# Performance work log

Measured on AMD Instinct MI355X. Metric: run time of the kernel, lower is better.

The kernel has to match this reference:

```python
import jax, jax.numpy as jnp
import numpy as np

N_NODES = 50000
N_EDGES = 800000
D = 96
DEPTH = 2


def setup_inputs() -> dict:
    key = jax.random.key(0)
    ks = jax.random.split(key, 8)
    scale = 1.0 / np.sqrt(D)
    x = jax.random.normal(ks[0], (N_NODES, D), dtype=jnp.float32)
    W0 = jax.random.normal(ks[1], (DEPTH, D, D), dtype=jnp.float32) * scale
    b0 = jnp.zeros((DEPTH, D), dtype=jnp.float32)
    W1 = jax.random.normal(ks[2], (DEPTH, D, D), dtype=jnp.float32) * scale
    b1 = jnp.zeros((DEPTH, D), dtype=jnp.float32)
    W2 = jax.random.normal(ks[3], (DEPTH, 2 * D, D), dtype=jnp.float32) * (1.0 / np.sqrt(2 * D))
    b2 = jnp.zeros((DEPTH, D), dtype=jnp.float32)
    edge_src = jax.random.randint(ks[4], (N_EDGES,), 0, N_NODES, dtype=jnp.int64 if jax.config.jax_enable_x64 else jnp.int32)
    edge_dst = jnp.sort(jax.random.randint(ks[5], (N_EDGES,), 0, N_NODES, dtype=jnp.int64 if jax.config.jax_enable_x64 else jnp.int32))
    return {"x": x, "W0": W0, "b0": b0, "W1": W1, "b1": b1,
            "W2": W2, "b2": b2, "edge_src": edge_src, "edge_dst": edge_dst}


def reference(x, W0, b0, W1, b1, W2, b2, edge_src, edge_dst):
    # x: [N, D] node features; edge lists define sparse adjacency A (A[dst, src] = 1).
    n = x.shape[0]
    depth = W0.shape[0]
    for i in range(depth):
        h_self = x @ W1[i] + b1[i]                      # [N, D] self transform
        h_nb = x @ W0[i] + b0[i]                        # [N, D] neighbor transform
        # sparse.mm(A, h_nb): sum of h_nb over in-neighbors of each vertex
        agg = jax.ops.segment_sum(h_nb[edge_src], edge_dst, num_segments=n)  # [N, D]
        x = jnp.concatenate([h_self, agg], axis=-1) @ W2[i] + b2[i]          # [N, D]
        # torch.std uses unbiased estimator (ddof=1)
        x = x / jnp.std(x, axis=-1, ddof=1, keepdims=True)
    return x
```

## Files before the change

kernel.cpp:

```cpp
#include <hip/hip_runtime.h>
#include <hip/hip_bf16.h>

typedef __attribute__((ext_vector_type(8))) short short8;
typedef __attribute__((ext_vector_type(16))) float f32x16;

__device__ __forceinline__ float bf2f(unsigned short h){
  union{unsigned u; float f;} c; c.u = ((unsigned)h)<<16; return c.f;
}
__device__ __forceinline__ unsigned short f2bf(float f){
  union{float f; unsigned u;} c; c.f = f;
  return (unsigned short)((c.u + 0x7fffu + ((c.u>>16)&1u))>>16);
}

__global__ void k_wc(const float* __restrict__ W0, const float* __restrict__ W1,
                     const float* __restrict__ W2, unsigned short* __restrict__ WcF){
  int b = blockIdx.x;
  int i = b / 192, k = b % 192, c = threadIdx.x;
  const float* w2 = W2 + (size_t)i*192*96;
  float s = 0.f;
  if (k < 96){
    const float* w1 = W1 + (size_t)i*96*96 + (size_t)k*96;
    for (int j=0;j<96;++j) s += w1[j] * w2[j*96 + c];
  } else {
    const float* w0 = W0 + (size_t)i*96*96 + (size_t)(k-96)*96;
    for (int j=0;j<96;++j) s += w0[j] * w2[(96+j)*96 + c];
  }
  int kt = k >> 4, hfk = (k >> 3) & 1, j = k & 7;
  int t = c >> 5, cl = c & 31;
  WcF[(size_t)((i*12 + kt)*3 + t)*512 + (size_t)(hfk*32 + cl)*8 + j] = f2bf(s);
}

__global__ void k_bias(const float* __restrict__ b0, const float* __restrict__ b1,
                       const float* __restrict__ b2, const float* __restrict__ W2,
                       float* __restrict__ cvec, float* __restrict__ dvec){
  int i = blockIdx.x, c = threadIdx.x;
  const float* w2 = W2 + (size_t)i*192*96;
  float s = b2[i*96+c], d = 0.f;
  for (int j=0;j<96;++j){
    s += b1[i*96+j] * w2[j*96 + c];
    d += b0[i*96+j] * w2[(96+j)*96 + c];
  }
  cvec[i*96+c] = s; dvec[i*96+c] = d;
}

__global__ void k_cast(const float* __restrict__ x, unsigned short* __restrict__ xb, int total4){
  int idx = blockIdx.x*blockDim.x + threadIdx.x;
  if (idx >= total4) return;
  float4 v = reinterpret_cast<const float4*>(x)[idx];
  ushort4 o; o.x = f2bf(v.x); o.y = f2bf(v.y); o.z = f2bf(v.z); o.w = f2bf(v.w);
  reinterpret_cast<ushort4*>(xb)[idx] = o;
}

__global__ void k_rowptr(const int* __restrict__ dst, int nE, int* __restrict__ rs, int nN){
  int n = blockIdx.x*blockDim.x + threadIdx.x;
  if (n > nN) return;
  int lo = 0, hi = nE;
  while (lo < hi){ int mid = (lo+hi)>>1; if (dst[mid] < n) lo = mid+1; else hi = mid; }
  rs[n] = lo;
}

__device__ __forceinline__ void acc8(float* a, uint4 v){
  a[0] += bf2f((unsigned short)(v.x & 0xffffu));
  a[1] += bf2f((unsigned short)(v.x >> 16));
  a[2] += bf2f((unsigned short)(v.y & 0xffffu));
  a[3] += bf2f((unsigned short)(v.y >> 16));
  a[4] += bf2f((unsigned short)(v.z & 0xffffu));
  a[5] += bf2f((unsigned short)(v.z >> 16));
  a[6] += bf2f((unsigned short)(v.w & 0xffffu));
  a[7] += bf2f((unsigned short)(v.w >> 16));
}

__global__ __launch_bounds__(192) void k_agg(
    const unsigned short* __restrict__ xb, const int* __restrict__ esrc,
    const int* __restrict__ rs, unsigned short* __restrict__ xa,
    int* __restrict__ deg, int nN)
{
  int n = blockIdx.x*16 + threadIdx.y;
  if (n >= nN) return;
  const int q = threadIdx.x;
  const unsigned short* xq = xb + q*8;
  const int e0 = rs[n], e1 = rs[n+1];
  if (q == 0) deg[n] = e1 - e0;

  float a[8] = {0,0,0,0,0,0,0,0};

  int e = e0;
  for (; e+8 <= e1; e += 8){
    int s0 = esrc[e],   s1 = esrc[e+1], s2 = esrc[e+2], s3 = esrc[e+3];
    int s4 = esrc[e+4], s5 = esrc[e+5], s6 = esrc[e+6], s7 = esrc[e+7];
    uint4 v0 = *reinterpret_cast<const uint4*>(xq + (size_t)s0*96);
    uint4 v1 = *reinterpret_cast<const uint4*>(xq + (size_t)s1*96);
    uint4 v2 = *reinterpret_cast<const uint4*>(xq + (size_t)s2*96);
    uint4 v3 = *reinterpret_cast<const uint4*>(xq + (size_t)s3*96);
    uint4 v4 = *reinterpret_cast<const uint4*>(xq + (size_t)s4*96);
    uint4 v5 = *reinterpret_cast<const uint4*>(xq + (size_t)s5*96);
    uint4 v6 = *reinterpret_cast<const uint4*>(xq + (size_t)s6*96);
    uint4 v7 = *reinterpret_cast<const uint4*>(xq + (size_t)s7*96);
    acc8(a, v0); acc8(a, v1); acc8(a, v2); acc8(a, v3);
    acc8(a, v4); acc8(a, v5); acc8(a, v6); acc8(a, v7);
  }
  for (; e+4 <= e1; e += 4){
    int s0 = esrc[e], s1 = esrc[e+1], s2 = esrc[e+2], s3 = esrc[e+3];
    uint4 v0 = *reinterpret_cast<const uint4*>(xq + (size_t)s0*96);
    uint4 v1 = *reinterpret_cast<const uint4*>(xq + (size_t)s1*96);
    uint4 v2 = *reinterpret_cast<const uint4*>(xq + (size_t)s2*96);
    uint4 v3 = *reinterpret_cast<const uint4*>(xq + (size_t)s3*96);
    acc8(a, v0); acc8(a, v1); acc8(a, v2); acc8(a, v3);
  }
  for (; e < e1; ++e){
    int s = esrc[e];
    uint4 v = *reinterpret_cast<const uint4*>(xq + (size_t)s*96);
    acc8(a, v);
  }

  uint4 o;
  o.x = (unsigned)f2bf(a[0]) | ((unsigned)f2bf(a[1]) << 16);
  o.y = (unsigned)f2bf(a[2]) | ((unsigned)f2bf(a[3]) << 16);
  o.z = (unsigned)f2bf(a[4]) | ((unsigned)f2bf(a[5]) << 16);
  o.w = (unsigned)f2bf(a[6]) | ((unsigned)f2bf(a[7]) << 16);
  *reinterpret_cast<uint4*>(xa + (size_t)n*96 + q*8) = o;
}

template<int LAST>
__global__ __launch_bounds__(256) void k_gemm(
    const unsigned short* __restrict__ xb, const unsigned short* __restrict__ xav,
    const unsigned short* __restrict__ WcF, const float* __restrict__ cvec,
    const float* __restrict__ dvec, const int* __restrict__ deg,
    float* __restrict__ outf, unsigned short* __restrict__ outb, int nN)
{
  const int wid = (blockIdx.x<<2) + (threadIdx.x>>6);
  const int nstrips = (nN+31)>>5;
  if (wid >= nstrips) return;
  const int lane = threadIdx.x & 63;
  const int cl = lane & 31;
  const int hf = lane >> 5;
  const int row0 = wid << 5;
  int arow = row0 + cl; if (arow >= nN) arow = nN-1;

  const short8* xr = reinterpret_cast<const short8*>(xb  + (size_t)arow*96);
  const short8* ar = reinterpret_cast<const short8*>(xav + (size_t)arow*96);
  const short8* wf = reinterpret_cast<const short8*>(WcF);

  short8 afr[12];
  #pragma unroll
  for (int kt=0; kt<6; ++kt){ afr[kt] = xr[kt*2 + hf]; afr[6+kt] = ar[kt*2 + hf]; }

  f32x16 acc[3];
  #pragma unroll
  for (int t=0;t<3;++t){
    #pragma unroll
    for (int i=0;i<16;++i) acc[t][i] = 0.f;
  }

  #pragma unroll
  for (int kt=0; kt<12; ++kt){
    short8 a = afr[kt];
    #pragma unroll
    for (int t=0;t<3;++t){
      short8 b = wf[(kt*3+t)*64 + lane];
      acc[t] = __builtin_amdgcn_mfma_f32_32x32x16_bf16(a, b, acc[t], 0, 0, 0);
    }
  }

  float cv[3], dv[3];
  #pragma unroll
  for (int t=0;t<3;++t){ cv[t] = cvec[t*32+cl]; dv[t] = dvec[t*32+cl]; }

  #pragma unroll
  for (int r=0;r<16;++r){
    const int rl = (r&3) + ((r>>2)<<3) + (hf<<2);
    const int rg = row0 + rl;
    const int rgc = rg < nN ? rg : nN-1;
    const float dgv = (float)deg[rgc];
    float v0 = acc[0][r] + cv[0] + dgv*dv[0];
    float v1 = acc[1][r] + cv[1] + dgv*dv[1];
    float v2 = acc[2][r] + cv[2] + dgv*dv[2];
    float s  = v0+v1+v2;
    float s2 = v0*v0 + v1*v1 + v2*v2;
    #pragma unroll
    for (int m=1;m<32;m<<=1){ s += __shfl_xor(s,m,64); s2 += __shfl_xor(s2,m,64); }
    float var = (s2 - s*s*(1.0f/96.0f)) * (1.0f/95.0f);
    float sc  = 1.0f / sqrtf(var);
    if (rg < nN){
      if (LAST){
        float* o = outf + (size_t)rg*96;
        o[cl] = v0*sc; o[32+cl] = v1*sc; o[64+cl] = v2*sc;
      } else {
        unsigned short* o = outb + (size_t)rg*96;
        o[cl] = f2bf(v0*sc); o[32+cl] = f2bf(v1*sc); o[64+cl] = f2bf(v2*sc);
      }
    }
  }
}

extern "C" void kernel_launch(void* const* d_in, const int* in_sizes, int n_in,
                              void* d_out, int out_size, void* d_ws, size_t ws_size,
                              hipStream_t stream)
{
  const float* x   = (const float*)d_in[0];
  const float* W0  = (const float*)d_in[1];
  const float* b0  = (const float*)d_in[2];
  const float* W1  = (const float*)d_in[3];
  const float* b1  = (const float*)d_in[4];
  const float* W2  = (const float*)d_in[5];
  const float* b2  = (const float*)d_in[6];
  const int* esrc  = (const int*)d_in[7];
  const int* edst  = (const int*)d_in[8];
  const int nN = in_sizes[0] / 96;
  const int nE = in_sizes[7];
  const int depth = in_sizes[1] / (96*96);
  float* out = (float*)d_out;

  char* p = (char*)d_ws;
  auto alloc = [&](size_t bytes)->char*{ char* r = p; p += (bytes + 255) & ~(size_t)255; return r; };
  unsigned short* WcF  = (unsigned short*)alloc((size_t)depth*12*3*512*2);
  float* cvec          = (float*)alloc((size_t)depth*96*4);
  float* dvec          = (float*)alloc((size_t)depth*96*4);
  int* rs              = (int*)alloc((size_t)(nN+1)*4);
  int* deg             = (int*)alloc((size_t)nN*4);
  unsigned short* xb0  = (unsigned short*)alloc((size_t)nN*96*2);
  unsigned short* xb1  = (unsigned short*)alloc((size_t)nN*96*2);
  unsigned short* xav  = (unsigned short*)alloc((size_t)nN*96*2);

  k_wc<<<dim3(depth*192), dim3(96), 0, stream>>>(W0, W1, W2, WcF);
  k_bias<<<dim3(depth), dim3(96), 0, stream>>>(b0, b1, b2, W2, cvec, dvec);
  int tot4 = nN*96/4;
  k_cast<<<dim3((tot4+255)/256), dim3(256), 0, stream>>>(x, xb0, tot4);
  k_rowptr<<<dim3((nN+1+255)/256), dim3(256), 0, stream>>>(edst, nE, rs, nN);

  const int aggGrid  = (nN+15)/16;
  const int gemmGrid = (((nN+31)/32)+3)/4;

  unsigned short* cur = xb0;
  unsigned short* nxt = xb1;
  for (int i=0; i<depth; ++i){
    k_agg<<<dim3(aggGrid), dim3(12,16), 0, stream>>>(cur, esrc, rs, xav, deg, nN);
    if (i == depth-1){
      k_gemm<1><<<dim3(gemmGrid), dim3(256), 0, stream>>>(
          cur, xav, WcF + (size_t)i*12*3*512, cvec + i*96, dvec + i*96, deg,
          out, (unsigned short*)nullptr, nN);
    } else {
      k_gemm<0><<<dim3(gemmGrid), dim3(256), 0, stream>>>(
          cur, xav, WcF + (size_t)i*12*3*512, cvec + i*96, dvec + i*96, deg,
          (float*)nullptr, nxt, nN);
      unsigned short* t = cur; cur = nxt; nxt = t;
    }
  }
}
```

Before: 183.3 us.

## Store GEMM A-operands in MFMA fragment layout and fuse prep kernels

Adds fragment-ordered copies of node features (xf) and aggregates (xaf) so each GEMM wave loads its A fragments with fully coalesced per-lane reads instead of strided row reads. The aggregation kernel now writes its output directly in fragment order. The weight and bias precompute kernels are merged, as are the cast and rowptr kernels, to cut launch count. The cost is an extra k_frag pass between layers that rewrites the new features into fragment layout, plus a duplicate write in the cast step.

```diff
diff --git a/kernel.cpp b/kernel.cpp
--- a/kernel.cpp
+++ b/kernel.cpp
@@ -12,51 +12,77 @@
   return (unsigned short)((c.u + 0x7fffu + ((c.u>>16)&1u))>>16);
 }
 
-__global__ void k_wc(const float* __restrict__ W0, const float* __restrict__ W1,
-                     const float* __restrict__ W2, unsigned short* __restrict__ WcF){
-  int b = blockIdx.x;
-  int i = b / 192, k = b % 192, c = threadIdx.x;
-  const float* w2 = W2 + (size_t)i*192*96;
-  float s = 0.f;
-  if (k < 96){
-    const float* w1 = W1 + (size_t)i*96*96 + (size_t)k*96;
-    for (int j=0;j<96;++j) s += w1[j] * w2[j*96 + c];
+
+__global__ void k_wcb(const float* __restrict__ W0, const float* __restrict__ W1,
+                      const float* __restrict__ W2, const float* __restrict__ b0,
+                      const float* __restrict__ b1, const float* __restrict__ b2,
+                      unsigned short* __restrict__ WcF, float* __restrict__ cvec,
+                      float* __restrict__ dvec, int depth){
+  int b = blockIdx.x, c = threadIdx.x;
+  int nwc = depth*192;
+  if (b < nwc){
+    int i = b/192, k = b%192;
+    const float* w  = (k<96) ? (W1 + (size_t)i*96*96 + (size_t)k*96)
+                             : (W0 + (size_t)i*96*96 + (size_t)(k-96)*96);
+    const float* w2 = W2 + (size_t)i*192*96 + (k<96 ? 0 : 96*96);
+    float s0=0.f,s1=0.f,s2=0.f,s3=0.f;
+    for (int j=0;j<96;j+=4){
+      s0 += w[j]   * w2[(j)*96 + c];
+      s1 += w[j+1] * w2[(j+1)*96 + c];
+      s2 += w[j+2] * w2[(j+2)*96 + c];
+      s3 += w[j+3] * w2[(j+3)*96 + c];
+    }
+    float s = (s0+s1)+(s2+s3);
+    int kt = k>>4, hfk=(k>>3)&1, jj=k&7;
+    int t=c>>5, cl=c&31;
+    WcF[(size_t)((i*12+kt)*3+t)*512 + (size_t)(hfk*32+cl)*8 + jj] = f2bf(s);
   } else {
-    const float* w0 = W0 + (size_t)i*96*96 + (size_t)(k-96)*96;
-    for (int j=0;j<96;++j) s += w0[j] * w2[(96+j)*96 + c];
-  }
-  int kt = k >> 4, hfk = (k >> 3) & 1, j = k & 7;
-  int t = c >> 5, cl = c & 31;
-  WcF[(size_t)((i*12 + kt)*3 + t)*512 + (size_t)(hfk*32 + cl)*8 + j] = f2bf(s);
-}
-
-__global__ void k_bias(const float* __restrict__ b0, const float* __restrict__ b1,
-                       const float* __restrict__ b2, const float* __restrict__ W2,
-                       float* __restrict__ cvec, float* __restrict__ dvec){
-  int i = blockIdx.x, c = threadIdx.x;
-  const float* w2 = W2 + (size_t)i*192*96;
-  float s = b2[i*96+c], d = 0.f;
-  for (int j=0;j<96;++j){
-    s += b1[i*96+j] * w2[j*96 + c];
-    d += b0[i*96+j] * w2[(96+j)*96 + c];
-  }
-  cvec[i*96+c] = s; dvec[i*96+c] = d;
-}
-
-__global__ void k_cast(const float* __restrict__ x, unsigned short* __restrict__ xb, int total4){
-  int idx = blockIdx.x*blockDim.x + threadIdx.x;
-  if (idx >= total4) return;
-  float4 v = reinterpret_cast<const float4*>(x)[idx];
-  ushort4 o; o.x = f2bf(v.x); o.y = f2bf(v.y); o.z = f2bf(v.z); o.w = f2bf(v.w);
-  reinterpret_cast<ushort4*>(xb)[idx] = o;
-}
-
-__global__ void k_rowptr(const int* __restrict__ dst, int nE, int* __restrict__ rs, int nN){
-  int n = blockIdx.x*blockDim.x + threadIdx.x;
-  if (n > nN) return;
-  int lo = 0, hi = nE;
-  while (lo < hi){ int mid = (lo+hi)>>1; if (dst[mid] < n) lo = mid+1; else hi = mid; }
-  rs[n] = lo;
+    int i = b - nwc;
+    const float* w2 = W2 + (size_t)i*192*96;
+    float s = b2[i*96+c], d=0.f;
+    for (int j=0;j<96;++j){
+      s += b1[i*96+j]*w2[j*96+c];
+      d += b0[i*96+j]*w2[(96+j)*96+c];
+    }
+    cvec[i*96+c]=s; dvec[i*96+c]=d;
+  }
+}
+
+__global__ __launch_bounds__(256) void k_prep(
+    const float* __restrict__ x, unsigned short* __restrict__ xb,
+    unsigned short* __restrict__ xf, const int* __restrict__ dst, int nE,
+    int* __restrict__ rs, int nN, int castBlocks){
+  if ((int)blockIdx.x < castBlocks){
+    int tid = blockIdx.x*256 + threadIdx.x;
+    if (tid >= nN*12) return;
+    int n = tid/12, q = tid%12;
+    const float4* src = reinterpret_cast<const float4*>(x + (size_t)n*96 + q*8);
+    float4 f0 = src[0], f1 = src[1];
+    uint4 o;
+    o.x = (unsigned)f2bf(f0.x) | ((unsigned)f2bf(f0.y)<<16);
+    o.y = (unsigned)f2bf(f0.z) | ((unsigned)f2bf(f0.w)<<16);
+    o.z = (unsigned)f2bf(f1.x) | ((unsigned)f2bf(f1.y)<<16);
+    o.w = (unsigned)f2bf(f1.z) | ((unsigned)f2bf(f1.w)<<16);
+    *reinterpret_cast<uint4*>(xb + (size_t)n*96 + q*8) = o;
+    int strip=n>>5, cl=n&31, kt=q>>1, hf=q&1;
+    *reinterpret_cast<uint4*>(xf + ((size_t)(strip*6+kt)*64 + hf*32+cl)*8) = o;
+  } else {
+    int n = ((int)blockIdx.x - castBlocks)*256 + threadIdx.x;
+    if (n > nN) return;
+    int lo=0, hi=nE;
+    while(lo<hi){int mid=(lo+hi)>>1; if(dst[mid]<n) lo=mid+1; else hi=mid;}
+    rs[n]=lo;
+  }
+}
+
+__global__ __launch_bounds__(256) void k_frag(
+    const unsigned short* __restrict__ xb, unsigned short* __restrict__ xf, int nN){
+  int tid = blockIdx.x*256+threadIdx.x;
+  if (tid >= nN*12) return;
+  int n=tid/12, q=tid%12;
+  uint4 v = *reinterpret_cast<const uint4*>(xb + (size_t)n*96 + q*8);
+  int strip=n>>5, cl=n&31, kt=q>>1, hf=q&1;
+  *reinterpret_cast<uint4*>(xf + ((size_t)(strip*6+kt)*64 + hf*32+cl)*8) = v;
 }
 
 __device__ __forceinline__ void acc8(float* a, uint4 v){
@@ -72,7 +98,7 @@
 
 __global__ __launch_bounds__(192) void k_agg(
     const unsigned short* __restrict__ xb, const int* __restrict__ esrc,
-    const int* __restrict__ rs, unsigned short* __restrict__ xa,
+    const int* __restrict__ rs, unsigned short* __restrict__ xaf,
     int* __restrict__ deg, int nN)
 {
   int n = blockIdx.x*16 + threadIdx.y;
@@ -118,12 +144,13 @@
   o.y = (unsigned)f2bf(a[2]) | ((unsigned)f2bf(a[3]) << 16);
   o.z = (unsigned)f2bf(a[4]) | ((unsigned)f2bf(a[5]) << 16);
   o.w = (unsigned)f2bf(a[6]) | ((unsigned)f2bf(a[7]) << 16);
-  *reinterpret_cast<uint4*>(xa + (size_t)n*96 + q*8) = o;
+  int strip=n>>5, cl=n&31, kt=q>>1, hf=q&1;
+  *reinterpret_cast<uint4*>(xaf + ((size_t)(strip*6+kt)*64 + hf*32+cl)*8) = o;
 }
 
 template<int LAST>
 __global__ __launch_bounds__(256) void k_gemm(
-    const unsigned short* __restrict__ xb, const unsigned short* __restrict__ xav,
+    const unsigned short* __restrict__ xf, const unsigned short* __restrict__ xaf,
     const unsigned short* __restrict__ WcF, const float* __restrict__ cvec,
     const float* __restrict__ dvec, const int* __restrict__ deg,
     float* __restrict__ outf, unsigned short* __restrict__ outb, int nN)
@@ -135,15 +162,14 @@
   const int cl = lane & 31;
   const int hf = lane >> 5;
   const int row0 = wid << 5;
-  int arow = row0 + cl; if (arow >= nN) arow = nN-1;
-
-  const short8* xr = reinterpret_cast<const short8*>(xb  + (size_t)arow*96);
-  const short8* ar = reinterpret_cast<const short8*>(xav + (size_t)arow*96);
-  const short8* wf = reinterpret_cast<const short8*>(WcF);
+
+  const short8* xfp = reinterpret_cast<const short8*>(xf)  + (size_t)wid*6*64;
+  const short8* xap = reinterpret_cast<const short8*>(xaf) + (size_t)wid*6*64;
+  const short8* wf  = reinterpret_cast<const short8*>(WcF);
 
   short8 afr[12];
   #pragma unroll
-  for (int kt=0; kt<6; ++kt){ afr[kt] = xr[kt*2 + hf]; afr[6+kt] = ar[kt*2 + hf]; }
+  for (int kt=0; kt<6; ++kt){ afr[kt] = xfp[kt*64 + lane]; afr[6+kt] = xap[kt*64 + lane]; }
 
   f32x16 acc[3];
   #pragma unroll
@@ -211,6 +237,8 @@
   const int depth = in_sizes[1] / (96*96);
   float* out = (float*)d_out;
 
+  const int nstrips = (nN+31)/32;
+
   char* p = (char*)d_ws;
   auto alloc = [&](size_t bytes)->char*{ char* r = p; p += (bytes + 255) & ~(size_t)255; return r; };
   unsigned short* WcF  = (unsigned short*)alloc((size_t)depth*12*3*512*2);
@@ -220,29 +248,32 @@
   int* deg             = (int*)alloc((size_t)nN*4);
   unsigned short* xb0  = (unsigned short*)alloc((size_t)nN*96*2);
   unsigned short* xb1  = (unsigned short*)alloc((size_t)nN*96*2);
-  unsigned short* xav  = (unsigned short*)alloc((size_t)nN*96*2);
-
-  k_wc<<<dim3(depth*192), dim3(96), 0, stream>>>(W0, W1, W2, WcF);
-  k_bias<<<dim3(depth), dim3(96), 0, stream>>>(b0, b1, b2, W2, cvec, dvec);
-  int tot4 = nN*96/4;
-  k_cast<<<dim3((tot4+255)/256), dim3(256), 0, stream>>>(x, xb0, tot4);
-  k_rowptr<<<dim3((nN+1+255)/256), dim3(256), 0, stream>>>(edst, nE, rs, nN);
+  unsigned short* xf   = (unsigned short*)alloc((size_t)nstrips*3072*2);
+  unsigned short* xaf  = (unsigned short*)alloc((size_t)nstrips*3072*2);
+
+  k_wcb<<<dim3(depth*192+depth), dim3(96), 0, stream>>>(W0, W1, W2, b0, b1, b2,
+                                                        WcF, cvec, dvec, depth);
+  const int castBlocks = (nN*12+255)/256;
+  const int rpBlocks   = (nN+1+255)/256;
+  k_prep<<<dim3(castBlocks+rpBlocks), dim3(256), 0, stream>>>(x, xb0, xf, edst, nE, rs, nN, castBlocks);
 
   const int aggGrid  = (nN+15)/16;
-  const int gemmGrid = (((nN+31)/32)+3)/4;
+  const int gemmGrid = (nstrips+3)/4;
+  const int fragGrid = castBlocks;
 
   unsigned short* cur = xb0;
   unsigned short* nxt = xb1;
   for (int i=0; i<depth; ++i){
-    k_agg<<<dim3(aggGrid), dim3(12,16), 0, stream>>>(cur, esrc, rs, xav, deg, nN);
+    k_agg<<<dim3(aggGrid), dim3(12,16), 0, stream>>>(cur, esrc, rs, xaf, deg, nN);
     if (i == depth-1){
       k_gemm<1><<<dim3(gemmGrid), dim3(256), 0, stream>>>(
-          cur, xav, WcF + (size_t)i*12*3*512, cvec + i*96, dvec + i*96, deg,
+          xf, xaf, WcF + (size_t)i*12*3*512, cvec + i*96, dvec + i*96, deg,
           out, (unsigned short*)nullptr, nN);
     } else {
       k_gemm<0><<<dim3(gemmGrid), dim3(256), 0, stream>>>(
-          cur, xav, WcF + (size_t)i*12*3*512, cvec + i*96, dvec + i*96, deg,
+          xf, xaf, WcF + (size_t)i*12*3*512, cvec + i*96, dvec + i*96, deg,
           (float*)nullptr, nxt, nN);
+      k_frag<<<dim3(fragGrid), dim3(256), 0, stream>>>(nxt, xf, nN);
       unsigned short* t = cur; cur = nxt; nxt = t;
     }
   }
```

Result: no change. 185.3 us (+1.1%).
